# Kernel tuning notes

Measured on AMD Instinct MI355X. Metric: run time of the kernel, lower is better.

Reference implementation:

```python
import jax, jax.numpy as jnp
import numpy as np

FP8_MAX = 448.0  # torch.finfo(float8_e4m3fn).max


def quant_fp8(x):
    # dynamic per-tensor quantization: amax -> scale -> cast to fp8
    amax = jnp.max(jnp.abs(x)).astype(jnp.float32)
    scale = jnp.minimum(FP8_MAX / jnp.maximum(amax, 1e-12), FP8_MAX)
    x_fp8 = jnp.clip(x * scale, -FP8_MAX, FP8_MAX).astype(jnp.float8_e4m3fn)
    return x_fp8, 1.0 / scale  # (fp8 data, dequant scale)


def setup_inputs() -> dict:
    key = jax.random.key(0)
    k1, k2, k3 = jax.random.split(key, 3)
    B, S, IN, OUT = 4, 8192, 1024, 1024
    input = jax.random.normal(k1, (B, S, IN), dtype=jnp.float32)
    # kaiming_uniform_(a=sqrt(5)) -> uniform(-1/sqrt(in), 1/sqrt(in))
    bound = 1.0 / np.sqrt(IN)
    weight = jax.random.uniform(k2, (OUT, IN), dtype=jnp.float32, minval=-bound, maxval=bound)
    bias = jax.random.uniform(k3, (OUT,), dtype=jnp.float32, minval=-bound, maxval=bound)
    return {"input": input, "weight": weight, "bias": bias}


def reference(input, weight, bias):
    prev_shape = input.shape
    x2d = input.reshape(-1, weight.shape[1])  # [T, in]
    w_fp8, w_scale = quant_fp8(weight)
    x_fp8, x_scale = quant_fp8(x2d)
    # bias add, bf16 output
    acc = jnp.matmul(x_fp8.astype(jnp.float32), w_fp8.astype(jnp.float32).T)
    out2d = (acc * (x_scale * w_scale) + bias).astype(jnp.bfloat16)
    out = out2d.reshape(*prev_shape[:-1], weight.shape[0]).astype(input.dtype)
    return out
```

## Files before the change

### kernel.cpp

```cpp
#include <hip/hip_runtime.h>
#include <hip/hip_bf16.h>

typedef float f32x4 __attribute__((ext_vector_type(4)));
typedef long lx2 __attribute__((ext_vector_type(2)));

#define FP8_MAX_F 448.0f

__device__ __forceinline__ float wave_max(float m) {
#pragma unroll
    for (int off = 32; off > 0; off >>= 1)
        m = fmaxf(m, __shfl_xor(m, off));
    return m;
}

__global__ void amax2_kernel(const float* __restrict__ x, long nx,
                             const float* __restrict__ w, long nw,
                             float* __restrict__ px, float* __restrict__ pw,
                             int ga) {
    __shared__ float red[4];
    const float* src; long n; float* dst; int bid, blocks;
    if ((int)blockIdx.x < ga) { src = x; n = nx; dst = px; bid = blockIdx.x; blocks = ga; }
    else { src = w; n = nw; dst = pw; bid = blockIdx.x - ga; blocks = gridDim.x - ga; }

    const long stride = (long)blocks * blockDim.x * 16;
    long i = ((long)bid * blockDim.x + threadIdx.x) * 16;
    float m = 0.0f;
    for (; i < n; i += stride) {
        f32x4 v0 = *(const f32x4*)(src + i);
        f32x4 v1 = *(const f32x4*)(src + i + 4);
        f32x4 v2 = *(const f32x4*)(src + i + 8);
        f32x4 v3 = *(const f32x4*)(src + i + 12);
        float m0 = fmaxf(fmaxf(fabsf(v0.x), fabsf(v0.y)), fmaxf(fabsf(v0.z), fabsf(v0.w)));
        float m1 = fmaxf(fmaxf(fabsf(v1.x), fabsf(v1.y)), fmaxf(fabsf(v1.z), fabsf(v1.w)));
        float m2 = fmaxf(fmaxf(fabsf(v2.x), fabsf(v2.y)), fmaxf(fabsf(v2.z), fabsf(v2.w)));
        float m3 = fmaxf(fmaxf(fabsf(v3.x), fabsf(v3.y)), fmaxf(fabsf(v3.z), fabsf(v3.w)));
        m = fmaxf(m, fmaxf(fmaxf(m0, m1), fmaxf(m2, m3)));
    }
    m = wave_max(m);
    const int wave = threadIdx.x >> 6;
    if ((threadIdx.x & 63) == 0) red[wave] = m;
    __syncthreads();
    if (threadIdx.x == 0)
        dst[bid] = fmaxf(fmaxf(red[0], red[1]), fmaxf(red[2], red[3]));
}

__global__ void amax_final_kernel(const float* __restrict__ px, int npx,
                                  const float* __restrict__ pw, int npw,
                                  unsigned* __restrict__ amax) {
    __shared__ float red[4];
    const float* p; int n;
    if (blockIdx.x == 0) { p = px; n = npx; } else { p = pw; n = npw; }
    float m = 0.0f;
    for (int i = threadIdx.x; i < n; i += blockDim.x) m = fmaxf(m, p[i]);
    m = wave_max(m);
    const int wave = threadIdx.x >> 6;
    if ((threadIdx.x & 63) == 0) red[wave] = m;
    __syncthreads();
    if (threadIdx.x == 0) {
        m = fmaxf(fmaxf(red[0], red[1]), fmaxf(red[2], red[3]));
        amax[blockIdx.x] = __float_as_uint(m);
    }
}

__global__ void quant2_kernel(const float* __restrict__ x, long nx8,
                              const float* __restrict__ w, long nw8,
                              const unsigned* __restrict__ amax_bits,
                              unsigned* __restrict__ qx, unsigned* __restrict__ qw,
                              int ga) {
    const float* src; long n8; unsigned* q; int bid, blocks; float a;
    if ((int)blockIdx.x < ga) { src = x; n8 = nx8; q = qx; bid = blockIdx.x; blocks = ga;
                                a = __uint_as_float(amax_bits[0]); }
    else { src = w; n8 = nw8; q = qw; bid = blockIdx.x - ga; blocks = gridDim.x - ga;
           a = __uint_as_float(amax_bits[1]); }
    const float scale = fminf(FP8_MAX_F / fmaxf(a, 1e-12f), FP8_MAX_F);

    const long stride = (long)blocks * blockDim.x;
    for (long i = (long)bid * blockDim.x + threadIdx.x; i < n8; i += stride) {
        f32x4 v0 = *(const f32x4*)(src + i * 8);
        f32x4 v1 = *(const f32x4*)(src + i * 8 + 4);
        float c0 = fminf(fmaxf(v0.x * scale, -FP8_MAX_F), FP8_MAX_F);
        float c1 = fminf(fmaxf(v0.y * scale, -FP8_MAX_F), FP8_MAX_F);
        float c2 = fminf(fmaxf(v0.z * scale, -FP8_MAX_F), FP8_MAX_F);
        float c3 = fminf(fmaxf(v0.w * scale, -FP8_MAX_F), FP8_MAX_F);
        float c4 = fminf(fmaxf(v1.x * scale, -FP8_MAX_F), FP8_MAX_F);
        float c5 = fminf(fmaxf(v1.y * scale, -FP8_MAX_F), FP8_MAX_F);
        float c6 = fminf(fmaxf(v1.z * scale, -FP8_MAX_F), FP8_MAX_F);
        float c7 = fminf(fmaxf(v1.w * scale, -FP8_MAX_F), FP8_MAX_F);
        int r0 = __builtin_amdgcn_cvt_pk_fp8_f32(c0, c1, 0, false);
        r0 = __builtin_amdgcn_cvt_pk_fp8_f32(c2, c3, r0, true);
        int r1 = __builtin_amdgcn_cvt_pk_fp8_f32(c4, c5, 0, false);
        r1 = __builtin_amdgcn_cvt_pk_fp8_f32(c6, c7, r1, true);
        uint2 rr; rr.x = (unsigned)r0; rr.y = (unsigned)r1;
        *(uint2*)(q + i * 2) = rr;
    }
}

__global__ __launch_bounds__(512, 2) void gemm_fp8_kernel(
    const unsigned char* __restrict__ Xq,
    const unsigned char* __restrict__ Wq,
    const float* __restrict__ bias,
    const unsigned* __restrict__ amax_bits,
    float* __restrict__ out,
    int M, int N, int K, int nbn)
{
    __shared__ unsigned char ldsA[3][16384];
    __shared__ unsigned char ldsB[3][16384];

    const int tid  = threadIdx.x;
    const int lane = tid & 63;
    const int wave = tid >> 6;
    const int wm128 = (wave >> 2) * 128;
    const int wn64  = (wave & 3) * 64;

    const int l15 = lane & 15;
    const int lhi = lane >> 4;

    const int cpx = gridDim.x >> 3;
    const int wg  = ((int)blockIdx.x & 7) * cpx + ((int)blockIdx.x >> 3);
    const int bn = wg % nbn;
    const int bm = wg / nbn;
    const int rowStart = bm << 8;
    const int colStart = bn << 8;

    const int aoff0 = lhi * 4096 + (wm128 + l15) * 16;
    const int boff  = lhi * 4096 + (wn64 + l15) * 16;

    const size_t aoffs = (size_t)(rowStart + (tid & 255)) * K + (tid >> 8) * 16;
    const size_t boffs = (size_t)(colStart + (tid & 255)) * K + (tid >> 8) * 16;
    const int tid16 = tid * 16;

    f32x4 acc[8][4] = {};

#define STAGE_A(t, sl)                                                                          \
    do {                                                                                        \
        const size_t kk_ = (size_t)(t) * 64;                                                    \
        __builtin_amdgcn_global_load_lds(                                                       \
            (const __attribute__((address_space(1))) void*)(Xq + aoffs + kk_),                  \
            (__attribute__((address_space(3))) void*)(&ldsA[sl][tid16]), 16, 0, 0);             \
        __builtin_amdgcn_global_load_lds(                                                       \
            (const __attribute__((address_space(1))) void*)(Xq + aoffs + 32 + kk_),             \
            (__attribute__((address_space(3))) void*)(&ldsA[sl][8192 + tid16]), 16, 0, 0);      \
    } while (0)

#define STAGE_B(t, sl)                                                                          \
    do {                                                                                        \
        const size_t kk_ = (size_t)(t) * 64;                                                    \
        __builtin_amdgcn_global_load_lds(                                                       \
            (const __attribute__((address_space(1))) void*)(Wq + boffs + kk_),                  \
            (__attribute__((address_space(3))) void*)(&ldsB[sl][tid16]), 16, 0, 0);             \
        __builtin_amdgcn_global_load_lds(                                                       \
            (const __attribute__((address_space(1))) void*)(Wq + boffs + 32 + kk_),             \
            (__attribute__((address_space(3))) void*)(&ldsB[sl][8192 + tid16]), 16, 0, 0);      \
    } while (0)

#define MFMA16(AF, KS, MO)                                                                      \
    do {                                                                                        \
        __builtin_amdgcn_s_setprio(1);                                                          \
        _Pragma("unroll")                                                                       \
        for (int mi_ = 0; mi_ < 4; ++mi_)                                                       \
            _Pragma("unroll")                                                                   \
            for (int ni_ = 0; ni_ < 4; ++ni_)                                                   \
                acc[(MO) + mi_][ni_] = __builtin_amdgcn_mfma_f32_16x16x32_fp8_fp8(              \
                    AF[mi_][KS], bf[ni_][KS], acc[(MO) + mi_][ni_], 0, 0, 0);                   \
        __builtin_amdgcn_s_setprio(0);                                                          \
    } while (0)

#define BAR()  do { __builtin_amdgcn_s_barrier(); __builtin_amdgcn_sched_barrier(0); } while (0)
#define LGKM0() do { asm volatile("s_waitcnt lgkmcnt(0)" ::: "memory");                         \
                     __builtin_amdgcn_sched_barrier(0); } while (0)

    STAGE_A(0, 0); STAGE_B(0, 0);
    STAGE_A(1, 1); STAGE_B(1, 1);
    asm volatile("s_waitcnt vmcnt(4)" ::: "memory");
    __builtin_amdgcn_s_barrier();
    __builtin_amdgcn_sched_barrier(0);

    const int nT = K >> 6;
    int s = 0;
#pragma unroll 1
    for (int t = 0; t < nT; ++t) {
        const unsigned char* bA = &ldsA[s][0];
        const unsigned char* bB = &ldsB[s][0];
        const int s2 = (s >= 1) ? (s - 1) : (s + 2);
        lx2 af[4], bf[4], ag[4];

#pragma unroll
        for (int q_ = 0; q_ < 4; ++q_) {
            bf[q_] = *(const lx2*)(bB + boff + q_ * 256);
            af[q_] = *(const lx2*)(bA + aoff0 + q_ * 256);
        }
        if (t + 2 < nT) STAGE_A(t + 2, s2);
        BAR();
        LGKM0();
        MFMA16(af, 0, 0);
        BAR();

#pragma unroll
        for (int q_ = 0; q_ < 4; ++q_)
            ag[q_] = *(const lx2*)(bA + aoff0 + 1024 + q_ * 256);
        if (t + 2 < nT) STAGE_B(t + 2, s2);
        BAR();
        MFMA16(af, 1, 0);
        BAR();

        LGKM0();
        MFMA16(ag, 0, 4);
        BAR();

        MFMA16(ag, 1, 4);
        if (t >= nT - 2) asm volatile("s_waitcnt vmcnt(0)" ::: "memory");
        else             asm volatile("s_waitcnt vmcnt(4)" ::: "memory");
        BAR();

        s = (s == 2) ? 0 : (s + 1);
    }
#undef STAGE_A
#undef STAGE_B
#undef MFMA16
#undef BAR
#undef LGKM0

    const float ax = __uint_as_float(amax_bits[0]);
    const float aw = __uint_as_float(amax_bits[1]);
    const float sx = fminf(FP8_MAX_F / fmaxf(ax, 1e-12f), FP8_MAX_F);
    const float sw = fminf(FP8_MAX_F / fmaxf(aw, 1e-12f), FP8_MAX_F);
    const float sc = (1.0f / sx) * (1.0f / sw);

    const int lhi4 = lhi * 4;
#pragma unroll
    for (int ni = 0; ni < 4; ++ni) {
        const int col = colStart + wn64 + ni * 16 + l15;
        const float bv = bias[col];
#pragma unroll
        for (int mi = 0; mi < 8; ++mi) {
            const size_t rbase = (size_t)(rowStart + wm128 + mi * 16 + lhi4) * N + col;
#pragma unroll
            for (int j = 0; j < 4; ++j) {
                float t = acc[mi][ni][j] * sc;
                t = t + bv;
                out[rbase + (size_t)j * N] = __bfloat162float(__float2bfloat16(t));
            }
        }
    }
}

extern "C" void kernel_launch(void* const* d_in, const int* in_sizes, int n_in,
                              void* d_out, int out_size, void* d_ws, size_t ws_size,
                              hipStream_t stream) {
    const float* input  = (const float*)d_in[0];
    const float* weight = (const float*)d_in[1];
    const float* bias   = (const float*)d_in[2];
    float* out = (float*)d_out;

    const int K = 1024;
    const int N = in_sizes[2];
    const long nX = in_sizes[0];
    const long nW = (long)N * K;
    const int M = (int)(nX / K);

    const int GA = 1984;
    const int GW = 64;

    unsigned char* ws = (unsigned char*)d_ws;
    unsigned* amax = (unsigned*)ws;
    unsigned char* Xq = ws + 256;
    unsigned char* Wq = Xq + (size_t)M * K;
    float* px = (float*)(Wq + (size_t)N * K);
    float* pw = px + GA;

    amax2_kernel<<<GA + GW, 256, 0, stream>>>(input, nX, weight, nW, px, pw, GA);
    amax_final_kernel<<<2, 256, 0, stream>>>(px, GA, pw, GW, amax);

    quant2_kernel<<<2048, 256, 0, stream>>>(input, nX / 8, weight, nW / 8, amax,
                                            (unsigned*)Xq, (unsigned*)Wq, GA);

    const int nbn = N / 256;
    const int nwg = (M / 256) * nbn;
    gemm_fp8_kernel<<<dim3(nwg), dim3(512), 0, stream>>>(Xq, Wq, bias, amax, out, M, N, K, nbn);
}
```

Before: 134.4 us.

## Software-pipeline LDS fragment loads with ping-pong registers and fewer barriers per K-tile

Restructures the GEMM main loop so the A/B register fragments for the next K-tile are prefetched from LDS while the current tile's MFMAs run. Two register sets alternate through a two-step unrolled loop. Both global-to-LDS stages are issued together, and the four barriers per tile become one, with lgkmcnt waits placed finely around the work. This aims to hide LDS latency and cut barrier stalls, at the cost of more live registers, which may lower occupancy. It also assumes nT is even.

```diff
diff --git a/kernel.cpp b/kernel.cpp
--- a/kernel.cpp
+++ b/kernel.cpp
@@ -153,21 +153,49 @@
             (__attribute__((address_space(3))) void*)(&ldsB[sl][8192 + tid16]), 16, 0, 0);      \
     } while (0)
 
-#define MFMA16(AF, KS, MO)                                                                      \
+#define MFMA32(AF, BF, MO)                                                                      \
     do {                                                                                        \
         __builtin_amdgcn_s_setprio(1);                                                          \
         _Pragma("unroll")                                                                       \
-        for (int mi_ = 0; mi_ < 4; ++mi_)                                                       \
+        for (int ks_ = 0; ks_ < 2; ++ks_)                                                       \
             _Pragma("unroll")                                                                   \
-            for (int ni_ = 0; ni_ < 4; ++ni_)                                                   \
-                acc[(MO) + mi_][ni_] = __builtin_amdgcn_mfma_f32_16x16x32_fp8_fp8(              \
-                    AF[mi_][KS], bf[ni_][KS], acc[(MO) + mi_][ni_], 0, 0, 0);                   \
+            for (int mi_ = 0; mi_ < 4; ++mi_)                                                   \
+                _Pragma("unroll")                                                               \
+                for (int ni_ = 0; ni_ < 4; ++ni_)                                               \
+                    acc[(MO) + mi_][ni_] = __builtin_amdgcn_mfma_f32_16x16x32_fp8_fp8(          \
+                        AF[mi_][ks_], BF[ni_][ks_], acc[(MO) + mi_][ni_], 0, 0, 0);             \
         __builtin_amdgcn_s_setprio(0);                                                          \
     } while (0)
 
-#define BAR()  do { __builtin_amdgcn_s_barrier(); __builtin_amdgcn_sched_barrier(0); } while (0)
-#define LGKM0() do { asm volatile("s_waitcnt lgkmcnt(0)" ::: "memory");                         \
-                     __builtin_amdgcn_sched_barrier(0); } while (0)
+#define BODY(t, sA, AF, BF, AF2, BF2)                                                           \
+    do {                                                                                        \
+        const int s_  = (sA);                                                                   \
+        const int s1_ = (s_ + 1 >= 3) ? s_ - 2 : s_ + 1;                                        \
+        const int s2_ = (s_ + 2 >= 3) ? s_ - 1 : s_ + 2;                                        \
+        const unsigned char* bA_ = &ldsA[s_][0];                                                \
+        _Pragma("unroll")                                                                       \
+        for (int q_ = 0; q_ < 4; ++q_)                                                          \
+            ag[q_] = *(const lx2*)(bA_ + aoff0 + 1024 + q_ * 256);                              \
+        if ((t) + 2 < nT) { STAGE_A((t) + 2, s2_); STAGE_B((t) + 2, s2_); }                     \
+        asm volatile("s_waitcnt lgkmcnt(4)" ::: "memory");       \
+        __builtin_amdgcn_sched_barrier(0);                                                      \
+        MFMA32(AF, BF, 0);                                                                      \
+        asm volatile("s_waitcnt lgkmcnt(0)" ::: "memory");       \
+        if ((t) + 2 < nT) asm volatile("s_waitcnt vmcnt(4)" ::: "memory");                      \
+        else              asm volatile("s_waitcnt vmcnt(0)" ::: "memory");                      \
+        __builtin_amdgcn_s_barrier();                                                           \
+        __builtin_amdgcn_sched_barrier(0);                                                      \
+        if ((t) + 1 < nT) {                                                                     \
+            const unsigned char* nA_ = &ldsA[s1_][0];                                           \
+            const unsigned char* nB_ = &ldsB[s1_][0];                                           \
+            _Pragma("unroll")                                                                   \
+            for (int q_ = 0; q_ < 4; ++q_) {                                                    \
+                AF2[q_] = *(const lx2*)(nA_ + aoff0 + q_ * 256);                                \
+                BF2[q_] = *(const lx2*)(nB_ + boff + q_ * 256);                                 \
+            }                                                                                   \
+        }                                                                                       \
+        MFMA32(ag, BF, 4);                                                                      \
+    } while (0)
 
     STAGE_A(0, 0); STAGE_B(0, 0);
     STAGE_A(1, 1); STAGE_B(1, 1);
@@ -175,50 +203,26 @@
     __builtin_amdgcn_s_barrier();
     __builtin_amdgcn_sched_barrier(0);
 
+    lx2 afA[4], bfA[4], afB[4], bfB[4], ag[4];
+#pragma unroll
+    for (int q_ = 0; q_ < 4; ++q_) {
+        afA[q_] = *(const lx2*)(&ldsA[0][aoff0 + q_ * 256]);
+        bfA[q_] = *(const lx2*)(&ldsB[0][boff + q_ * 256]);
+    }
+
     const int nT = K >> 6;
     int s = 0;
 #pragma unroll 1
-    for (int t = 0; t < nT; ++t) {
-        const unsigned char* bA = &ldsA[s][0];
-        const unsigned char* bB = &ldsB[s][0];
-        const int s2 = (s >= 1) ? (s - 1) : (s + 2);
-        lx2 af[4], bf[4], ag[4];
-
-#pragma unroll
-        for (int q_ = 0; q_ < 4; ++q_) {
-            bf[q_] = *(const lx2*)(bB + boff + q_ * 256);
-            af[q_] = *(const lx2*)(bA + aoff0 + q_ * 256);
-        }
-        if (t + 2 < nT) STAGE_A(t + 2, s2);
-        BAR();
-        LGKM0();
-        MFMA16(af, 0, 0);
-        BAR();
-
-#pragma unroll
-        for (int q_ = 0; q_ < 4; ++q_)
-            ag[q_] = *(const lx2*)(bA + aoff0 + 1024 + q_ * 256);
-        if (t + 2 < nT) STAGE_B(t + 2, s2);
-        BAR();
-        MFMA16(af, 1, 0);
-        BAR();
-
-        LGKM0();
-        MFMA16(ag, 0, 4);
-        BAR();
-
-        MFMA16(ag, 1, 4);
-        if (t >= nT - 2) asm volatile("s_waitcnt vmcnt(0)" ::: "memory");
-        else             asm volatile("s_waitcnt vmcnt(4)" ::: "memory");
-        BAR();
-
-        s = (s == 2) ? 0 : (s + 1);
-    }
+    for (int t = 0; t < nT; t += 2) {
+        const int sn = (s + 1 >= 3) ? s - 2 : s + 1;
+        BODY(t,     s,  afA, bfA, afB, bfB);
+        BODY(t + 1, sn, afB, bfB, afA, bfA);
+        s = (s + 2 >= 3) ? s - 1 : s + 2;
+    }
+#undef BODY
+#undef MFMA32
 #undef STAGE_A
 #undef STAGE_B
-#undef MFMA16
-#undef BAR
-#undef LGKM0
 
     const float ax = __uint_as_float(amax_bits[0]);
     const float aw = __uint_as_float(amax_bits[1]);
```

Measured after the change: 128.4 us. 1.05x faster.
